# Optimization experiments

Measured on AMD Instinct MI355X. Metric: run time of the kernel, lower is better.

Reference implementation:

```python
import jax, jax.numpy as jnp
import numpy as np

N_NODES = 40000
N_EDGES = 640000
D = 128
N_GRAPHS = 64


def gcn_conv(x, W, b, edge_index):
    """PyG-style GCNConv: add self-loops, symmetric norm, linear, scatter-add."""
    n = x.shape[0]
    loops = jnp.arange(n, dtype=edge_index.dtype)
    src = jnp.concatenate([edge_index[0], loops])  # message sources (x_j)
    dst = jnp.concatenate([edge_index[1], loops])  # aggregation targets
    # deg computed over targets (col) with unit edge weights, incl. self-loops
    deg = jax.ops.segment_sum(jnp.ones_like(src, dtype=x.dtype), dst, num_segments=n)
    dinv = jnp.where(deg > 0, jax.lax.rsqrt(jnp.maximum(deg, 1.0)), 0.0)
    norm = dinv[src] * dinv[dst]  # [E+N]
    h = x @ W  # [N, d_out]
    out = jax.ops.segment_sum(norm[:, None] * h[src], dst, num_segments=n)
    return out + b


def global_mean_pool(x, batch, num_graphs):
    summed = jax.ops.segment_sum(x, batch, num_segments=num_graphs)
    counts = jax.ops.segment_sum(jnp.ones((x.shape[0],), x.dtype), batch, num_segments=num_graphs)
    return summed / jnp.maximum(counts, 1.0)[:, None]


def setup_inputs() -> dict:
    key = jax.random.key(0)
    ks = jax.random.split(key, 6)
    x = jax.random.normal(ks[0], (N_NODES, D), dtype=jnp.float32)
    edge_index = jax.random.randint(ks[1], (2, N_EDGES), 0, N_NODES)
    batch = jnp.sort(jax.random.randint(ks[2], (N_NODES,), 0, N_GRAPHS))
    s = 1.0 / np.sqrt(D)
    W1 = jax.random.normal(ks[3], (D, D), dtype=jnp.float32) * s
    W2 = jax.random.normal(ks[4], (D, D), dtype=jnp.float32) * s
    b1 = jnp.zeros((D,), jnp.float32)
    b2 = jnp.zeros((D,), jnp.float32)
    return {"x": x, "edge_index": edge_index, "batch": batch,
            "W1": W1, "b1": b1, "W2": W2, "b2": b2}


def reference(x, edge_index, batch, W1, b1, W2, b2):
    h = jax.nn.relu(gcn_conv(x, W1, b1, edge_index))
    h = gcn_conv(h, W2, b2, edge_index)  # no ReLU on last layer
    return global_mean_pool(h, batch, N_GRAPHS)
```

## Files before the change

### kernel.cpp

```cpp
#include <hip/hip_runtime.h>

#define D 128
#define N_GRAPHS 64

typedef unsigned int uint32;
typedef __attribute__((ext_vector_type(8))) _Float16 f16x8;
typedef __attribute__((ext_vector_type(4))) float f32x4;

__device__ __forceinline__ float hl(uint32 u) {
    return (float)__builtin_bit_cast(_Float16, (unsigned short)(u & 0xFFFF));
}
__device__ __forceinline__ float hh(uint32 u) {
    return (float)__builtin_bit_cast(_Float16, (unsigned short)(u >> 16));
}
__device__ __forceinline__ uint32 h2pair(float a, float b) {
    unsigned short ua = __builtin_bit_cast(unsigned short, (_Float16)a);
    unsigned short ub = __builtin_bit_cast(unsigned short, (_Float16)b);
    return (uint32)ua | ((uint32)ub << 16);
}


__global__ void count_rank_kernel(const int* __restrict__ dst, int* __restrict__ cnt,
                                  int* __restrict__ rank, int E) {
    int e = blockIdx.x * blockDim.x + threadIdx.x;
    if (e < E) rank[e] = atomicAdd(&cnt[dst[e]], 1);
}

__global__ __launch_bounds__(1024) void scanA_kernel(const int* __restrict__ cnt,
                                                     int* __restrict__ rowptr,
                                                     int* __restrict__ tot,
                                                     float* __restrict__ dinv,
                                                     float* __restrict__ c,
                                                     const int* __restrict__ batch, int n) {
    __shared__ int swave[16];
    int t = threadIdx.x;
    int lane = t & 63, wave = t >> 6;
    int i = blockIdx.x * 1024 + t;
    {
        size_t f4base = (size_t)blockIdx.x * 1024 * 16;
        size_t f4lim = (size_t)n * 16;
        float4 z = make_float4(0.f, 0.f, 0.f, 0.f);
#pragma unroll
        for (int q = 0; q < 16; ++q) {
            size_t idx = f4base + (size_t)q * 1024 + t;
            if (idx < f4lim) ((float4*)c)[idx] = z;
        }
    }
    int orig = (i < n) ? cnt[i] : 0;
    int v = orig;
#pragma unroll
    for (int off = 1; off < 64; off <<= 1) {
        int u = __shfl_up(v, off, 64);
        if (lane >= off) v += u;
    }
    if (lane == 63) swave[wave] = v;
    __syncthreads();
    if (wave == 0) {
        int wv = (lane < 16) ? swave[lane] : 0;
#pragma unroll
        for (int off = 1; off < 16; off <<= 1) {
            int u = __shfl_up(wv, off, 64);
            if (lane >= off) wv += u;
        }
        if (lane < 16) swave[lane] = wv;
    }
    if (i < n) {
        float dv = rsqrtf((float)(orig + 1));
        dinv[i] = dv;
        c[(size_t)i * N_GRAPHS + batch[i]] = dv * dv;
    }
    __syncthreads();
    int incl = v + ((wave > 0) ? swave[wave - 1] : 0);
    if (i < n) rowptr[i] = incl - orig;
    if (t == 1023) tot[blockIdx.x] = incl;
}

__global__ __launch_bounds__(1024) void scanB_kernel(int* __restrict__ rowptr,
                                                     const int* __restrict__ tot,
                                                     int n, int nchunks) {
    __shared__ int soff;
    int b = blockIdx.x, t = threadIdx.x;
    if (t == 0) {
        int o = 0;
        for (int j = 0; j < b; ++j) o += tot[j];
        soff = o;
    }
    __syncthreads();
    int i = b * 1024 + t;
    if (i < n) rowptr[i] += soff;
    if (b == 0 && t == 0) {
        int o = 0;
        for (int j = 0; j < nchunks; ++j) o += tot[j];
        rowptr[n] = o;
    }
}

__global__ void fill_kernel(const int* __restrict__ src, const int* __restrict__ dst,
                            const int* __restrict__ rowptr, const int* __restrict__ rank,
                            int* __restrict__ col,
                            const float* __restrict__ dinv,
                            float* __restrict__ c, const int* __restrict__ batch, int E) {
    int e = blockIdx.x * blockDim.x + threadIdx.x;
    if (e < E) {
        int s = src[e], d = dst[e];
        int pos = rowptr[d] + rank[e];
        col[pos] = s;
        float w = dinv[s] * dinv[d];
        atomicAdd(&c[(size_t)s * N_GRAPHS + batch[d]], w);
    }
}


#define GBM 64

__global__ __launch_bounds__(256) void mfma_gemm_kernel(const float* __restrict__ A,
                                                        const float* __restrict__ W,
                                                        uint32* __restrict__ hb, int M) {
    __shared__ uint32 lds[64 * 68 + 128 * 68];
    uint32* As = lds;
    uint32* Wt = lds + 64 * 68;
    int tid = threadIdx.x;
    int row0 = blockIdx.x * GBM;

#pragma unroll
    for (int j = 0; j < 8; ++j) {
        int idx = tid + j * 256;
        int r = idx >> 5, c4 = idx & 31;
        float4 v = make_float4(0.f, 0.f, 0.f, 0.f);
        if (row0 + r < M) v = *(const float4*)&A[(size_t)(row0 + r) * D + c4 * 4];
        As[r * 68 + c4 * 2 + 0] = h2pair(v.x, v.y);
        As[r * 68 + c4 * 2 + 1] = h2pair(v.z, v.w);
    }
    {
        int nn = tid & 127, half = tid >> 7;
        int kbase = half * 64;
#pragma unroll
        for (int kk = 0; kk < 64; kk += 2) {
            float v0 = W[(size_t)(kbase + kk) * D + nn];
            float v1 = W[(size_t)(kbase + kk + 1) * D + nn];
            Wt[nn * 68 + ((kbase + kk) >> 1)] = h2pair(v0, v1);
        }
    }
    __syncthreads();

    int wave = tid >> 6, lane = tid & 63;
    int quad = lane >> 4, l16 = lane & 15;
    int wr = (wave & 1) * 32;
    int wc = (wave >> 1) * 64;
    f32x4 acc[2][4];
#pragma unroll
    for (int mi = 0; mi < 2; ++mi)
#pragma unroll
        for (int ni = 0; ni < 4; ++ni) acc[mi][ni] = (f32x4){0.f, 0.f, 0.f, 0.f};

#pragma unroll
    for (int ks = 0; ks < 4; ++ks) {
        int kd = ks * 16 + quad * 4;
        f16x8 a0 = *(f16x8*)&As[(wr + l16) * 68 + kd];
        f16x8 a1 = *(f16x8*)&As[(wr + 16 + l16) * 68 + kd];
        f16x8 b0 = *(f16x8*)&Wt[(wc + l16) * 68 + kd];
        f16x8 b1 = *(f16x8*)&Wt[(wc + 16 + l16) * 68 + kd];
        f16x8 b2 = *(f16x8*)&Wt[(wc + 32 + l16) * 68 + kd];
        f16x8 b3 = *(f16x8*)&Wt[(wc + 48 + l16) * 68 + kd];
        acc[0][0] = __builtin_amdgcn_mfma_f32_16x16x32_f16(a0, b0, acc[0][0], 0, 0, 0);
        acc[0][1] = __builtin_amdgcn_mfma_f32_16x16x32_f16(a0, b1, acc[0][1], 0, 0, 0);
        acc[0][2] = __builtin_amdgcn_mfma_f32_16x16x32_f16(a0, b2, acc[0][2], 0, 0, 0);
        acc[0][3] = __builtin_amdgcn_mfma_f32_16x16x32_f16(a0, b3, acc[0][3], 0, 0, 0);
        acc[1][0] = __builtin_amdgcn_mfma_f32_16x16x32_f16(a1, b0, acc[1][0], 0, 0, 0);
        acc[1][1] = __builtin_amdgcn_mfma_f32_16x16x32_f16(a1, b1, acc[1][1], 0, 0, 0);
        acc[1][2] = __builtin_amdgcn_mfma_f32_16x16x32_f16(a1, b2, acc[1][2], 0, 0, 0);
        acc[1][3] = __builtin_amdgcn_mfma_f32_16x16x32_f16(a1, b3, acc[1][3], 0, 0, 0);
    }
    __syncthreads();

    unsigned short* cs = (unsigned short*)lds;
#pragma unroll
    for (int mi = 0; mi < 2; ++mi)
#pragma unroll
        for (int ni = 0; ni < 4; ++ni)
#pragma unroll
            for (int r = 0; r < 4; ++r) {
                int row = wr + mi * 16 + quad * 4 + r;
                int col = wc + ni * 16 + l16;
                cs[row * 128 + col] =
                    __builtin_bit_cast(unsigned short, (_Float16)acc[mi][ni][r]);
            }
    __syncthreads();
#pragma unroll
    for (int j = 0; j < 4; ++j) {
        int idx = tid + j * 256;
        int r = idx >> 4, q = idx & 15;
        if (row0 + r < M)
            *(uint4*)&hb[(size_t)(row0 + r) * 64 + q * 4] = *(uint4*)&lds[r * 64 + q * 4];
    }
}


__global__ __launch_bounds__(128) void agg_kernel(const uint32* __restrict__ hb,
                                                  const int* __restrict__ rowptr,
                                                  const int* __restrict__ col,
                                                  const float* __restrict__ dinv,
                                                  const float* __restrict__ bias,
                                                  uint32* __restrict__ h1, int n) {
    int tid = threadIdx.x;
    int lane32 = tid & 31;
    int slot = tid >> 5;
    int node = blockIdx.x * 4 + slot;
    if (node >= n) return;
    const uint2* __restrict__ h2 = (const uint2*)hb;

    float di = dinv[node];
    float ws = di * di;
    uint2 su = h2[(size_t)node * 32 + lane32];
    float a0 = ws * hl(su.x), a1 = ws * hh(su.x);
    float a2 = ws * hl(su.y), a3 = ws * hh(su.y);

    int k = rowptr[node], end = rowptr[node + 1];
    for (; k + 8 <= end; k += 8) {
        uint2 v[8];
        float w[8];
#pragma unroll
        for (int j = 0; j < 8; ++j) {
            int s = col[k + j];
            w[j] = dinv[s] * di;
            v[j] = h2[(size_t)s * 32 + lane32];
        }
#pragma unroll
        for (int j = 0; j < 8; ++j) {
            a0 = fmaf(w[j], hl(v[j].x), a0);
            a1 = fmaf(w[j], hh(v[j].x), a1);
            a2 = fmaf(w[j], hl(v[j].y), a2);
            a3 = fmaf(w[j], hh(v[j].y), a3);
        }
    }
    for (; k < end; ++k) {
        int s = col[k];
        float w = dinv[s] * di;
        uint2 v = h2[(size_t)s * 32 + lane32];
        a0 = fmaf(w, hl(v.x), a0);
        a1 = fmaf(w, hh(v.x), a1);
        a2 = fmaf(w, hl(v.y), a2);
        a3 = fmaf(w, hh(v.y), a3);
    }

    float4 b4 = ((const float4*)bias)[lane32];
    a0 = fmaxf(a0 + b4.x, 0.f);
    a1 = fmaxf(a1 + b4.y, 0.f);
    a2 = fmaxf(a2 + b4.z, 0.f);
    a3 = fmaxf(a3 + b4.w, 0.f);
    uint2 o;
    o.x = h2pair(a0, a1);
    o.y = h2pair(a2, a3);
    ((uint2*)h1)[(size_t)node * 32 + lane32] = o;
}


#define GP_NB 256
#define GP_T 16

__global__ __launch_bounds__(256) void gp_kernel(const float* __restrict__ c,
                                                 const uint32* __restrict__ H1,
                                                 float* __restrict__ Ppart, int n) {
    __shared__ float sc[GP_T][N_GRAPHS];
    __shared__ uint32 sh[GP_T][64];
    int t = threadIdx.x;
    int b = blockIdx.x;
    int jpb = (n + GP_NB - 1) / GP_NB;
    int j0 = b * jpb;
    int j1 = min(j0 + jpb, n);
    int g0 = (t & 7) * 8;
    int f0 = (t >> 3) * 4;
    float acc[8][4];
#pragma unroll
    for (int a = 0; a < 8; ++a)
#pragma unroll
        for (int q = 0; q < 4; ++q) acc[a][q] = 0.f;

    for (int jt = j0; jt < j1; jt += GP_T) {
        int cnt = min(GP_T, j1 - jt);
        {
            int r = t >> 4, q = t & 15;
            float4 v = (r < cnt) ? *(const float4*)&c[(size_t)(jt + r) * N_GRAPHS + q * 4]
                                 : make_float4(0.f, 0.f, 0.f, 0.f);
            *(float4*)&sc[r][q * 4] = v;
        }
        {
            int r = t >> 4, q = t & 15;
            uint4 v = make_uint4(0, 0, 0, 0);
            if (r < cnt) v = *(const uint4*)&H1[(size_t)(jt + r) * 64 + q * 4];
            *(uint4*)&sh[r][q * 4] = v;
        }
        __syncthreads();
#pragma unroll
        for (int r = 0; r < GP_T; ++r) {
            float cw[8], hv[4];
            *(float4*)&cw[0] = *(float4*)&sc[r][g0];
            *(float4*)&cw[4] = *(float4*)&sc[r][g0 + 4];
            uint32 u0 = sh[r][f0 >> 1], u1 = sh[r][(f0 >> 1) + 1];
            hv[0] = hl(u0); hv[1] = hh(u0); hv[2] = hl(u1); hv[3] = hh(u1);
#pragma unroll
            for (int a = 0; a < 8; ++a)
#pragma unroll
                for (int q = 0; q < 4; ++q) acc[a][q] = fmaf(cw[a], hv[q], acc[a][q]);
        }
        __syncthreads();
    }
    float* P = &Ppart[(size_t)b * N_GRAPHS * D];
#pragma unroll
    for (int a = 0; a < 8; ++a)
        *(float4*)&P[(size_t)(g0 + a) * D + f0] =
            make_float4(acc[a][0], acc[a][1], acc[a][2], acc[a][3]);
}

__global__ __launch_bounds__(128) void out_kernel(const float* __restrict__ Ppart,
                                                  const float* __restrict__ W2,
                                                  const float* __restrict__ b2,
                                                  const int* __restrict__ batch, int n,
                                                  float* __restrict__ out) {
    __shared__ float gs[D];
    __shared__ float srinv;
    int g = blockIdx.x, f = threadIdx.x;
    if (f == 0) {
        int lo = 0, hi = n;
        while (lo < hi) { int mid = (lo + hi) >> 1; if (batch[mid] < g) lo = mid + 1; else hi = mid; }
        int lb = lo;
        int g1 = g + 1;
        lo = 0; hi = n;
        while (lo < hi) { int mid = (lo + hi) >> 1; if (batch[mid] < g1) lo = mid + 1; else hi = mid; }
        int cg = lo - lb;
        srinv = (cg > 0) ? 1.0f / (float)cg : 0.0f;
    }
    float s = 0.f;
    for (int b = 0; b < GP_NB; ++b) s += Ppart[((size_t)b * N_GRAPHS + g) * D + f];
    gs[f] = s;
    __syncthreads();
    float acc = 0.f;
#pragma unroll 8
    for (int k = 0; k < D; ++k) acc = fmaf(gs[k], W2[k * D + f], acc);
    float r = srinv;
    out[g * D + f] = (r > 0.f) ? fmaf(acc, r, b2[f]) : 0.f;
}


extern "C" void kernel_launch(void* const* d_in, const int* in_sizes, int n_in,
                              void* d_out, int out_size, void* d_ws, size_t ws_size,
                              hipStream_t stream) {
    const float* x  = (const float*)d_in[0];
    const int*   ei = (const int*)d_in[1];
    const int*   batch = (const int*)d_in[2];
    const float* W1 = (const float*)d_in[3];
    const float* b1 = (const float*)d_in[4];
    const float* W2 = (const float*)d_in[5];
    const float* b2 = (const float*)d_in[6];
    float* out = (float*)d_out;

    const int n = in_sizes[2];
    const int E = in_sizes[1] / 2;
    const int* src = ei;
    const int* dst = ei + E;

    char* ws = (char*)d_ws;
    size_t off = 0;
    auto carve = [&](size_t bytes) {
        size_t o = off;
        off = (off + bytes + 255) & ~(size_t)255;
        return (void*)(ws + o);
    };
    int*    cnt    = (int*)carve((size_t)n * 4);
    int*    rowptr = (int*)carve((size_t)(n + 1) * 4);
    float*  dinv   = (float*)carve((size_t)n * 4);
    int*    col    = (int*)carve((size_t)E * 4);
    uint32* hb     = (uint32*)carve((size_t)n * D * 2);
    uint32* h1     = (uint32*)carve((size_t)n * D * 2);
    float*  c      = (float*)carve((size_t)n * N_GRAPHS * 4);
    int*    tot    = (int*)carve(64 * 4);
    int*    rank   = (int*)hb;
    float*  Ppart  = (float*)hb;
    (void)ws_size;

    const int nchunks = (n + 1023) >> 10;

    hipMemsetAsync(cnt, 0, (size_t)n * 4, stream);

    count_rank_kernel<<<(E + 255) / 256, 256, 0, stream>>>(dst, cnt, rank, E);
    scanA_kernel<<<nchunks, 1024, 0, stream>>>(cnt, rowptr, tot, dinv, c, batch, n);
    scanB_kernel<<<nchunks, 1024, 0, stream>>>(rowptr, tot, n, nchunks);
    fill_kernel<<<(E + 255) / 256, 256, 0, stream>>>(src, dst, rowptr, rank, col, dinv, c, batch, E);

    mfma_gemm_kernel<<<(n + GBM - 1) / GBM, 256, 0, stream>>>(x, W1, hb, n);
    agg_kernel<<<(n + 3) / 4, 128, 0, stream>>>(hb, rowptr, col, dinv, b1, h1, n);

    gp_kernel<<<GP_NB, 256, 0, stream>>>(c, h1, Ppart, n);
    out_kernel<<<N_GRAPHS, 128, 0, stream>>>(Ppart, W2, b2, batch, n, out);
}
```

Measured before the change: 226.5 us.

## Fuse CSR fill with GEMM launch, prepack W1 to fp16, split out_kernel work

Replaces the cnt memset with a prep kernel that also converts W1 to a transposed fp16 layout once. The fill and GEMM work now run as two block ranges of one launch, so the two independent stages overlap and one launch disappears. GEMM blocks read W from global or cache instead of rebuilding it in LDS per block, which also shrinks LDS use. The rank array gets its own buffer because hb is written concurrently. out_kernel uses 256 threads, with the reduction and matvec split across two halves.

```diff
diff --git a/kernel.cpp b/kernel.cpp
--- a/kernel.cpp
+++ b/kernel.cpp
@@ -17,6 +17,21 @@
     unsigned short ua = __builtin_bit_cast(unsigned short, (_Float16)a);
     unsigned short ub = __builtin_bit_cast(unsigned short, (_Float16)b);
     return (uint32)ua | ((uint32)ub << 16);
+}
+
+__global__ __launch_bounds__(256) void prep_kernel(int* __restrict__ cnt,
+                                                   const float* __restrict__ W1,
+                                                   uint32* __restrict__ Wh, int n) {
+    int i = blockIdx.x * 256 + threadIdx.x;
+    if (i < n) {
+        cnt[i] = 0;
+    } else if (i < n + D * (D / 2)) {
+        int j = i - n;
+        int nn = j & 127, kd = j >> 7;
+        float v0 = W1[(size_t)(2 * kd) * D + nn];
+        float v1 = W1[(size_t)(2 * kd + 1) * D + nn];
+        Wh[nn * 64 + kd] = h2pair(v0, v1);
+    }
 }
 
 
@@ -95,30 +110,31 @@
     }
 }
 
-__global__ void fill_kernel(const int* __restrict__ src, const int* __restrict__ dst,
-                            const int* __restrict__ rowptr, const int* __restrict__ rank,
-                            int* __restrict__ col,
-                            const float* __restrict__ dinv,
-                            float* __restrict__ c, const int* __restrict__ batch, int E) {
-    int e = blockIdx.x * blockDim.x + threadIdx.x;
-    if (e < E) {
-        int s = src[e], d = dst[e];
-        int pos = rowptr[d] + rank[e];
-        col[pos] = s;
-        float w = dinv[s] * dinv[d];
-        atomicAdd(&c[(size_t)s * N_GRAPHS + batch[d]], w);
-    }
-}
-
 
 #define GBM 64
 
-__global__ __launch_bounds__(256) void mfma_gemm_kernel(const float* __restrict__ A,
-                                                        const float* __restrict__ W,
-                                                        uint32* __restrict__ hb, int M) {
-    __shared__ uint32 lds[64 * 68 + 128 * 68];
+__global__ __launch_bounds__(256) void fill_gemm_kernel(
+    const float* __restrict__ A, const uint32* __restrict__ Wh,
+    uint32* __restrict__ hb, int M, int gemmBlocks,
+    const int* __restrict__ src, const int* __restrict__ dst,
+    const int* __restrict__ rowptr, const int* __restrict__ rank,
+    int* __restrict__ col, const float* __restrict__ dinv,
+    float* __restrict__ c, const int* __restrict__ batch, int E) {
+    __shared__ uint32 lds[64 * 68];
+
+    if (blockIdx.x >= gemmBlocks) {
+        int e = (blockIdx.x - gemmBlocks) * 256 + threadIdx.x;
+        if (e < E) {
+            int s = src[e], d = dst[e];
+            int pos = rowptr[d] + rank[e];
+            col[pos] = s;
+            float w = dinv[s] * dinv[d];
+            atomicAdd(&c[(size_t)s * N_GRAPHS + batch[d]], w);
+        }
+        return;
+    }
+
     uint32* As = lds;
-    uint32* Wt = lds + 64 * 68;
     int tid = threadIdx.x;
     int row0 = blockIdx.x * GBM;
 
@@ -131,16 +147,6 @@
         As[r * 68 + c4 * 2 + 0] = h2pair(v.x, v.y);
         As[r * 68 + c4 * 2 + 1] = h2pair(v.z, v.w);
     }
-    {
-        int nn = tid & 127, half = tid >> 7;
-        int kbase = half * 64;
-#pragma unroll
-        for (int kk = 0; kk < 64; kk += 2) {
-            float v0 = W[(size_t)(kbase + kk) * D + nn];
-            float v1 = W[(size_t)(kbase + kk + 1) * D + nn];
-            Wt[nn * 68 + ((kbase + kk) >> 1)] = h2pair(v0, v1);
-        }
-    }
     __syncthreads();
 
     int wave = tid >> 6, lane = tid & 63;
@@ -158,10 +164,10 @@
         int kd = ks * 16 + quad * 4;
         f16x8 a0 = *(f16x8*)&As[(wr + l16) * 68 + kd];
         f16x8 a1 = *(f16x8*)&As[(wr + 16 + l16) * 68 + kd];
-        f16x8 b0 = *(f16x8*)&Wt[(wc + l16) * 68 + kd];
-        f16x8 b1 = *(f16x8*)&Wt[(wc + 16 + l16) * 68 + kd];
-        f16x8 b2 = *(f16x8*)&Wt[(wc + 32 + l16) * 68 + kd];
-        f16x8 b3 = *(f16x8*)&Wt[(wc + 48 + l16) * 68 + kd];
+        f16x8 b0 = *(const f16x8*)&Wh[(wc + l16) * 64 + kd];
+        f16x8 b1 = *(const f16x8*)&Wh[(wc + 16 + l16) * 64 + kd];
+        f16x8 b2 = *(const f16x8*)&Wh[(wc + 32 + l16) * 64 + kd];
+        f16x8 b3 = *(const f16x8*)&Wh[(wc + 48 + l16) * 64 + kd];
         acc[0][0] = __builtin_amdgcn_mfma_f32_16x16x32_f16(a0, b0, acc[0][0], 0, 0, 0);
         acc[0][1] = __builtin_amdgcn_mfma_f32_16x16x32_f16(a0, b1, acc[0][1], 0, 0, 0);
         acc[0][2] = __builtin_amdgcn_mfma_f32_16x16x32_f16(a0, b2, acc[0][2], 0, 0, 0);
@@ -181,8 +187,8 @@
 #pragma unroll
             for (int r = 0; r < 4; ++r) {
                 int row = wr + mi * 16 + quad * 4 + r;
-                int col = wc + ni * 16 + l16;
-                cs[row * 128 + col] =
+                int col2 = wc + ni * 16 + l16;
+                cs[row * 128 + col2] =
                     __builtin_bit_cast(unsigned short, (_Float16)acc[mi][ni][r]);
             }
     __syncthreads();
@@ -312,15 +318,17 @@
             make_float4(acc[a][0], acc[a][1], acc[a][2], acc[a][3]);
 }
 
-__global__ __launch_bounds__(128) void out_kernel(const float* __restrict__ Ppart,
+__global__ __launch_bounds__(256) void out_kernel(const float* __restrict__ Ppart,
                                                   const float* __restrict__ W2,
                                                   const float* __restrict__ b2,
                                                   const int* __restrict__ batch, int n,
                                                   float* __restrict__ out) {
     __shared__ float gs[D];
+    __shared__ float part[2][D];
     __shared__ float srinv;
-    int g = blockIdx.x, f = threadIdx.x;
-    if (f == 0) {
+    int g = blockIdx.x, t = threadIdx.x;
+    int f = t & 127, half = t >> 7;
+    if (t == 0) {
         int lo = 0, hi = n;
         while (lo < hi) { int mid = (lo + hi) >> 1; if (batch[mid] < g) lo = mid + 1; else hi = mid; }
         int lb = lo;
@@ -331,14 +339,25 @@
         srinv = (cg > 0) ? 1.0f / (float)cg : 0.0f;
     }
     float s = 0.f;
-    for (int b = 0; b < GP_NB; ++b) s += Ppart[((size_t)b * N_GRAPHS + g) * D + f];
-    gs[f] = s;
+    int b0 = half * (GP_NB / 2);
+#pragma unroll 8
+    for (int b = b0; b < b0 + GP_NB / 2; ++b)
+        s += Ppart[((size_t)b * N_GRAPHS + g) * D + f];
+    part[half][f] = s;
+    __syncthreads();
+    if (half == 0) gs[f] = part[0][f] + part[1][f];
     __syncthreads();
     float acc = 0.f;
+    int k0 = half * (D / 2);
 #pragma unroll 8
-    for (int k = 0; k < D; ++k) acc = fmaf(gs[k], W2[k * D + f], acc);
-    float r = srinv;
-    out[g * D + f] = (r > 0.f) ? fmaf(acc, r, b2[f]) : 0.f;
+    for (int k = k0; k < k0 + D / 2; ++k) acc = fmaf(gs[k], W2[k * D + f], acc);
+    part[half][f] = acc;
+    __syncthreads();
+    if (half == 0) {
+        float a = part[0][f] + part[1][f];
+        float r = srinv;
+        out[g * D + f] = (r > 0.f) ? fmaf(a, r, b2[f]) : 0.f;
+    }
 }
 
 
@@ -374,22 +393,26 @@
     uint32* h1     = (uint32*)carve((size_t)n * D * 2);
     float*  c      = (float*)carve((size_t)n * N_GRAPHS * 4);
     int*    tot    = (int*)carve(64 * 4);
-    int*    rank   = (int*)hb;
+    int*    rank   = (int*)carve((size_t)E * 4);
+    uint32* Wh     = (uint32*)carve((size_t)D * (D / 2) * 4);
     float*  Ppart  = (float*)hb;
     (void)ws_size;
 
     const int nchunks = (n + 1023) >> 10;
 
-    hipMemsetAsync(cnt, 0, (size_t)n * 4, stream);
+    prep_kernel<<<(n + D * (D / 2) + 255) / 256, 256, 0, stream>>>(cnt, W1, Wh, n);
 
     count_rank_kernel<<<(E + 255) / 256, 256, 0, stream>>>(dst, cnt, rank, E);
     scanA_kernel<<<nchunks, 1024, 0, stream>>>(cnt, rowptr, tot, dinv, c, batch, n);
     scanB_kernel<<<nchunks, 1024, 0, stream>>>(rowptr, tot, n, nchunks);
-    fill_kernel<<<(E + 255) / 256, 256, 0, stream>>>(src, dst, rowptr, rank, col, dinv, c, batch, E);
-
-    mfma_gemm_kernel<<<(n + GBM - 1) / GBM, 256, 0, stream>>>(x, W1, hb, n);
+
+    const int gemmBlocks = (n + GBM - 1) / GBM;
+    const int fillBlocks = (E + 255) / 256;
+    fill_gemm_kernel<<<gemmBlocks + fillBlocks, 256, 0, stream>>>(
+        x, Wh, hb, n, gemmBlocks, src, dst, rowptr, rank, col, dinv, c, batch, E);
+
     agg_kernel<<<(n + 3) / 4, 128, 0, stream>>>(hb, rowptr, col, dinv, b1, h1, n);
 
     gp_kernel<<<GP_NB, 256, 0, stream>>>(c, h1, Ppart, n);
-    out_kernel<<<N_GRAPHS, 128, 0, stream>>>(Ppart, W2, b2, batch, n, out);
-}
+    out_kernel<<<N_GRAPHS, 256, 0, stream>>>(Ppart, W2, b2, batch, n, out);
+}
```

Measured after the change: 220.8 us. 2.5% less time.
